# Performance work log

Measured on AMD Instinct MI355X. Metric: run time of the kernel, lower is better.

The kernel has to match this reference:

```python
import jax, jax.numpy as jnp
import numpy as np

D_MODEL = 1024
H = 16
T = 1024
B = 8

def setup_inputs() -> dict:
    key = jax.random.key(0)
    k0, k1, k2, k3, k4 = jax.random.split(key, 5)
    return {
        "x": jax.random.normal(k0, (B, T, D_MODEL), dtype=jnp.float32),
        "Wq": jax.random.normal(k1, (D_MODEL, D_MODEL), dtype=jnp.float32),
        "Wk": jax.random.normal(k2, (D_MODEL, D_MODEL), dtype=jnp.float32),
        "Wv": jax.random.normal(k3, (D_MODEL, D_MODEL), dtype=jnp.float32),
        "Wp": jax.random.normal(k4, (D_MODEL, D_MODEL), dtype=jnp.float32),
    }

def reference(x, Wq, Wk, Wv, Wp):
    b, t, d = x.shape
    dh = d // H
    # projections
    q = (x @ Wq).reshape(b, t, H, dh)
    k = (x @ Wk).reshape(b, t, H, dh)
    v = (x @ Wv).reshape(b, t, H, dh)
    # [b, h, t, t] attention scores, scaled by sqrt(d_head)
    scores = jnp.einsum("bqhd,bkhd->bhqk", q, k) / jnp.sqrt(jnp.float32(dh))
    attn = jax.nn.softmax(scores, axis=-1)
    # [b, h, t, dh] -> [b, t, d]
    out = jnp.einsum("bhqk,bkhd->bqhd", attn, v).reshape(b, t, d)
    return out @ Wp
```

## Files before the change

### kernel.cpp

```cpp
#include <hip/hip_runtime.h>
#include <math.h>


typedef unsigned short u16;
typedef unsigned int u32;
typedef __bf16  bf16x8 __attribute__((ext_vector_type(8)));
typedef unsigned short u16x8 __attribute__((ext_vector_type(8)));
typedef unsigned short u16x4 __attribute__((ext_vector_type(4)));
typedef short s16x4 __attribute__((ext_vector_type(4)));
typedef unsigned int u32x2 __attribute__((ext_vector_type(2)));
typedef float f32x4 __attribute__((ext_vector_type(4)));

#define MFMA16(a,b,c) __builtin_amdgcn_mfma_f32_16x16x32_bf16((a),(b),(c),0,0,0)
#define MFMA16K16(a,b,c) __builtin_amdgcn_mfma_f32_16x16x16bf16_1k((a),(b),(c),0,0,0)

static __device__ __forceinline__ u16 f2b(float f){
  unsigned u = __builtin_bit_cast(unsigned, f);
  u += 0x7fffu + ((u >> 16) & 1u);
  return (u16)(u >> 16);
}
static __device__ __forceinline__ float b2f(u16 h){
  unsigned u = ((unsigned)h) << 16;
  return __builtin_bit_cast(float, u);
}
static __device__ __forceinline__ bf16x8 ldsfrag(const u16* p){
  return __builtin_bit_cast(bf16x8, *(const u16x8*)p);
}
static __device__ __forceinline__ u32 packhi(float fa, float fb){
  return __builtin_amdgcn_perm(__builtin_bit_cast(u32, fa),
                               __builtin_bit_cast(u32, fb), 0x07060302u);
}
static __device__ __forceinline__ void gld16(const void* g, void* l){
  __builtin_amdgcn_global_load_lds(
      (const __attribute__((address_space(1))) void*)g,
      (__attribute__((address_space(3))) void*)l, 16, 0, 0);
}


__global__ __launch_bounds__(256) void split_x_kernel(
    const float* __restrict__ x, u16* __restrict__ xh, u16* __restrict__ xl, int n)
{
  int i = (blockIdx.x * 256 + threadIdx.x) * 8;
  if (i >= n) return;
  float4 v0 = *(const float4*)(x + i);
  float4 v1 = *(const float4*)(x + i + 4);
  float vv[8] = {v0.x, v0.y, v0.z, v0.w, v1.x, v1.y, v1.z, v1.w};
  u16x8 hv, lv;
#pragma unroll
  for (int j = 0; j < 8; j++){
    u16 hb = f2b(vv[j]);
    hv[j] = hb;
    lv[j] = f2b(vv[j] - b2f(hb));
  }
  *(u16x8*)(xh + i) = hv;
  *(u16x8*)(xl + i) = lv;
}

__global__ __launch_bounds__(256) void transpose4_kernel(
    const float* __restrict__ Wq, const float* __restrict__ Wk,
    const float* __restrict__ Wv, const float* __restrict__ Wp,
    u16* __restrict__ qh_, u16* __restrict__ ql_,
    u16* __restrict__ kh_, u16* __restrict__ kl_,
    u16* __restrict__ vt_, u16* __restrict__ pt_)
{
  __shared__ float t[32][33];
  const int z = blockIdx.z;
  const float* W = (z == 0) ? Wq : (z == 1) ? Wk : (z == 2) ? Wv : Wp;
  u16* Th = (z == 0) ? qh_ : (z == 1) ? kh_ : (z == 2) ? vt_ : pt_;
  u16* Tl = (z == 0) ? ql_ : (z == 1) ? kl_ : nullptr;
  int n0 = blockIdx.x * 32, k0 = blockIdx.y * 32;
  int tx = threadIdx.x, ty = threadIdx.y;
#pragma unroll
  for (int i = 0; i < 4; i++){
    int k = k0 + ty + i * 8;
    t[ty + i * 8][tx] = W[(size_t)k * 1024 + n0 + tx];
  }
  __syncthreads();
#pragma unroll
  for (int i = 0; i < 4; i++){
    int n = n0 + ty + i * 8;
    float v = t[tx][ty + i * 8];
    u16 h = f2b(v);
    Th[(size_t)n * 1024 + k0 + tx] = h;
    if (Tl) Tl[(size_t)n * 1024 + k0 + tx] = f2b(v - b2f(h));
  }
}

template<int OUTMODE>
__global__ __launch_bounds__(256) void gemm_bt_kernel(
    const u16* __restrict__ A, const u16* __restrict__ Bt, void* __restrict__ Cv,
    int M, int N, int K)
{
  __shared__ __attribute__((aligned(16))) u16 lA[4096], lB[4096];
  const int tid = threadIdx.x, lane = tid & 63, wave = tid >> 6;
  const int quad = lane >> 4, l15 = lane & 15;
  const int row0 = blockIdx.x * 128, col0 = blockIdx.y * 128;
  const int wm = wave >> 1, wn = wave & 1;
  const int sr = lane >> 2, sc = (lane & 3) * 8;
  f32x4 acc[4][4];
#pragma unroll
  for (int mt = 0; mt < 4; mt++)
#pragma unroll
    for (int nt = 0; nt < 4; nt++) acc[mt][nt] = (f32x4)0.0f;

  for (int k0 = 0; k0 < K; k0 += 32){
#pragma unroll
    for (int i = 0; i < 2; i++){
      int c = wave * 2 + i;
      gld16(A  + (size_t)(row0 + c * 16 + sr) * K + k0 + sc, &lA[c * 512]);
      gld16(Bt + (size_t)(col0 + c * 16 + sr) * K + k0 + sc, &lB[c * 512]);
    }
    __syncthreads();
    bf16x8 a[4], b[4];
#pragma unroll
    for (int t = 0; t < 4; t++){
      a[t] = ldsfrag(&lA[(wm * 64 + t * 16 + l15) * 32 + quad * 8]);
      b[t] = ldsfrag(&lB[(wn * 64 + t * 16 + l15) * 32 + quad * 8]);
    }
#pragma unroll
    for (int mt = 0; mt < 4; mt++)
#pragma unroll
      for (int nt = 0; nt < 4; nt++)
        acc[mt][nt] = MFMA16(a[mt], b[nt], acc[mt][nt]);
    __syncthreads();
  }
  if (OUTMODE == 2){
#pragma unroll
    for (int mt = 0; mt < 4; mt++)
#pragma unroll
      for (int nt = 0; nt < 4; nt++){
        int row = row0 + wm * 64 + mt * 16 + quad * 4;
        int col = col0 + wn * 64 + nt * 16 + l15;
        int bb = row >> 10, tt = row & 1023;
        int hh = (col >> 6) & 15, d = col & 63;
        int bhI = bb * 16 + hh;
        int ktile = tt >> 7, fkt = (tt >> 4) & 7, qF = (tt >> 2) & 3;
        int nd = d >> 4, l15F = d & 15;
        size_t idx = ((((size_t)(bhI * 8 + ktile) * 8 + fkt) * 4 + nd) * 64
                      + qF * 16 + l15F) * 4;
        u16x4 vals;
#pragma unroll
        for (int r = 0; r < 4; r++) vals[r] = f2b(acc[mt][nt][r]);
        *(u16x4*)(((u16*)Cv) + idx) = vals;
      }
  } else {
#pragma unroll
    for (int mt = 0; mt < 4; mt++)
#pragma unroll
      for (int nt = 0; nt < 4; nt++)
#pragma unroll
        for (int r = 0; r < 4; r++){
          int row = row0 + wm * 64 + mt * 16 + quad * 4 + r;
          int col = col0 + wn * 64 + nt * 16 + l15;
          ((float*)Cv)[(size_t)row * N + col] = acc[mt][nt][r];
        }
  }
}

__global__ __launch_bounds__(512, 2) void gemm_qk_kernel(
    const u16* __restrict__ Ah, const u16* __restrict__ Al,
    const u16* __restrict__ Bh, const u16* __restrict__ Bl,
    u16* __restrict__ Qhf, u16* __restrict__ Qlf,
    u16* __restrict__ Khf, u16* __restrict__ Klf, int M, int N, int K)
{
  __shared__ __attribute__((aligned(16))) u16 sA[2][2][8192], sB[2][2][8192];
  const int tid = threadIdx.x, lane = tid & 63, wave = tid >> 6;
  const int quad = lane >> 4, l15 = lane & 15;
  const int wm = wave >> 2, wn = wave & 3;
  const int row0 = blockIdx.x * 256, col0 = blockIdx.y * 256;
  const int f0a = (wave & 3) | ((wave & 4) << 1);
  const int f0b = (wave & 1) | ((wave >> 1) << 2);
  const size_t fstride = (size_t)16 * K;
  const size_t abase = (size_t)(row0 + l15) * K + quad * 8;
  const size_t bbase = (size_t)(col0 + l15) * K + quad * 8;
  (void)M; (void)N;

  f32x4 acc[8][4];
#pragma unroll
  for (int mt = 0; mt < 8; mt++)
#pragma unroll
    for (int nt = 0; nt < 4; nt++) acc[mt][nt] = (f32x4)0.0f;

#define STAGE_G0(KK, NB) do {                                              \
    gld16(Ah + abase + (size_t)f0a * fstride + (KK), &sA[NB][0][f0a * 512]); \
    gld16(Al + abase + (size_t)f0a * fstride + (KK), &sA[NB][1][f0a * 512]); \
    gld16(Bh + bbase + (size_t)f0b * fstride + (KK), &sB[NB][0][f0b * 512]); \
    gld16(Bl + bbase + (size_t)f0b * fstride + (KK), &sB[NB][1][f0b * 512]); \
  } while (0)
#define STAGE_G1(KK, NB) do {                                                        \
    gld16(Bh + bbase + (size_t)(f0b + 2) * fstride + (KK), &sB[NB][0][(f0b + 2) * 512]); \
    gld16(Bl + bbase + (size_t)(f0b + 2) * fstride + (KK), &sB[NB][1][(f0b + 2) * 512]); \
  } while (0)
#define STAGE_G2(KK, NB) do {                                                        \
    gld16(Ah + abase + (size_t)(f0a + 4) * fstride + (KK), &sA[NB][0][(f0a + 4) * 512]); \
    gld16(Al + abase + (size_t)(f0a + 4) * fstride + (KK), &sA[NB][1][(f0a + 4) * 512]); \
  } while (0)
#define RD_A(B4, BUF) do {                                        \
    _Pragma("unroll")                                             \
    for (int i = 0; i < 4; i++){                                  \
      int fa = wm * 8 + (B4) + i;                                 \
      ahf[i] = ldsfrag(&sA[BUF][0][fa * 512 + lane * 8]);         \
      alf[i] = ldsfrag(&sA[BUF][1][fa * 512 + lane * 8]);         \
    } } while (0)
#define RD_B(B2, BUF) do {                                        \
    _Pragma("unroll")                                             \
    for (int j = 0; j < 2; j++){                                  \
      int fb = wn * 4 + (B2) + j;                                 \
      bhf[j] = ldsfrag(&sB[BUF][0][fb * 512 + lane * 8]);         \
      blf[j] = ldsfrag(&sB[BUF][1][fb * 512 + lane * 8]);         \
    } } while (0)
#define MM(M0, N0) do {                                                      \
    __builtin_amdgcn_s_setprio(1);                                           \
    _Pragma("unroll")                                                        \
    for (int i = 0; i < 4; i++)                                              \
      _Pragma("unroll")                                                      \
      for (int j = 0; j < 2; j++){                                           \
        acc[(M0) + i][(N0) + j] = MFMA16(alf[i], bhf[j], acc[(M0) + i][(N0) + j]); \
        acc[(M0) + i][(N0) + j] = MFMA16(ahf[i], blf[j], acc[(M0) + i][(N0) + j]); \
        acc[(M0) + i][(N0) + j] = MFMA16(ahf[i], bhf[j], acc[(M0) + i][(N0) + j]); \
      }                                                                      \
    __builtin_amdgcn_s_setprio(0);                                           \
  } while (0)
#define VMCNT4() asm volatile("s_waitcnt vmcnt(4)" ::: "memory")
#define VMCNT6() asm volatile("s_waitcnt vmcnt(6)" ::: "memory")
#define BARRIER() asm volatile("s_barrier" ::: "memory")

  const int NT = K >> 5;
  STAGE_G0(0, 0);
  STAGE_G1(0, 0);
  STAGE_G2(0, 0);

  bf16x8 ahf[4], alf[4], bhf[2], blf[2];
#pragma unroll 2
  for (int t = 0; t < NT; t++){
    const int buf = t & 1, nb = buf ^ 1;
    const int kn = ((t + 1) & (NT - 1)) * 32;
    VMCNT4();
    BARRIER();
    RD_A(0, buf);
    RD_B(0, buf);
    STAGE_G0(kn, nb);
    MM(0, 0);
    VMCNT6();
    BARRIER();
    RD_B(2, buf);
    STAGE_G1(kn, nb);
    MM(0, 2);
    VMCNT6();
    BARRIER();
    RD_A(4, buf);
    STAGE_G2(kn, nb);
    MM(4, 2);
    RD_B(0, buf);
    MM(4, 0);
  }
  asm volatile("s_waitcnt vmcnt(0)" ::: "memory");

#undef STAGE_G0
#undef STAGE_G1
#undef STAGE_G2
#undef RD_A
#undef RD_B
#undef MM
#undef VMCNT4
#undef VMCNT6
#undef BARRIER

  const bool isQ = (col0 < 1024);
#pragma unroll
  for (int mt = 0; mt < 8; mt++)
#pragma unroll
    for (int nt = 0; nt < 4; nt++)
#pragma unroll
      for (int r = 0; r < 4; r++){
        int row = row0 + wm * 128 + mt * 16 + quad * 4 + r;
        int col = col0 + wn * 64 + nt * 16 + l15;
        int bb = row >> 10, tt = row & 1023;
        int hh = (col >> 6) & 15, d = col & 63;
        int bhI = bb * 16 + hh;
        int kc = d >> 5, qF = (d >> 3) & 3, j = d & 7;
        float v = acc[mt][nt][r];
        u16 hi = f2b(v);
        u16 lo = f2b(v - b2f(hi));
        if (isQ){
          int qtile = tt >> 7, rr = tt & 127;
          int wv = rr >> 5, mtF = (rr >> 4) & 1, l15F = tt & 15;
          size_t idx = ((((size_t)(bhI * 8 + qtile) * 4 + wv) * 2 + mtF) * 2 + kc) * 512
                       + (qF * 16 + l15F) * 8 + j;
          Qhf[idx] = hi; Qlf[idx] = lo;
        } else {
          int ktile = tt >> 7, fkt = (tt >> 4) & 7, l15F = tt & 15;
          size_t idx = (((size_t)(bhI * 8 + ktile) * 8 + fkt) * 2 + kc) * 512
                       + (qF * 16 + l15F) * 8 + j;
          Khf[idx] = hi; Klf[idx] = lo;
        }
      }
}

__global__ __launch_bounds__(256, 3) void attn_kernel(
    const u16* __restrict__ Qhf, const u16* __restrict__ Qlf,
    const u16* __restrict__ Khf, const u16* __restrict__ Klf,
    const u16* __restrict__ Vf, u16* __restrict__ O)
{
  __shared__ __attribute__((aligned(16))) u16 lKh[2][4096], lKl[2][4096], lV[2][4096];
  const int tid = threadIdx.x, lane = tid & 63, wave = tid >> 6;
  const int quad = lane >> 4, l15 = lane & 15;
  const int qt = blockIdx.x >> 7, bh = blockIdx.x & 127;
  const int b = bh >> 4, h = bh & 15;
  const int q0 = qt * 128;
  const float BETA = 0.18033688011112042f;

  bf16x8 qh[2][2], ql[2][2];
  {
    size_t qbase = (size_t)(bh * 8 + qt) * 8192 + wave * 2048 + lane * 8;
    u16* sh = &lKh[0][0];  u16* sl = &lKl[0][0];
#pragma unroll
    for (int i = 0; i < 4; i++){
      gld16(Qhf + qbase + i * 512, sh + wave * 2048 + i * 512);
      gld16(Qlf + qbase + i * 512, sl + wave * 2048 + i * 512);
    }
    __syncthreads();
#pragma unroll
    for (int mt = 0; mt < 2; mt++)
#pragma unroll
      for (int kc = 0; kc < 2; kc++){
        int off = wave * 2048 + (mt * 2 + kc) * 512 + lane * 8;
        qh[mt][kc] = ldsfrag(sh + off);
        ql[mt][kc] = ldsfrag(sl + off);
      }
    __syncthreads();
  }

  float m_i[2] = {-3.0e38f, -3.0e38f}, l_i[2] = {0.0f, 0.0f};
  f32x4 o_acc[2][4];
#pragma unroll
  for (int mt = 0; mt < 2; mt++)
#pragma unroll
    for (int nd = 0; nd < 4; nd++) o_acc[mt][nd] = (f32x4)0.0f;

  const size_t pan = (size_t)bh * 65536;
#pragma unroll
  for (int i = 0; i < 2; i++){
    int c = wave * 2 + i;
    gld16(Khf + pan + c * 512 + lane * 8, &lKh[0][c * 512]);
    gld16(Klf + pan + c * 512 + lane * 8, &lKl[0][c * 512]);
    gld16(Vf  + pan + c * 512 + lane * 8, &lV [0][c * 512]);
  }

#pragma unroll 1
  for (int j = 0; j < 16; j++){
    const int cur = j & 1;
    __syncthreads();
    if (j < 15){
      size_t nb = pan + (size_t)(j + 1) * 4096;
      const int nxt = cur ^ 1;
#pragma unroll
      for (int i = 0; i < 2; i++){
        int c = wave * 2 + i;
        gld16(Khf + nb + c * 512 + lane * 8, &lKh[nxt][c * 512]);
        gld16(Klf + nb + c * 512 + lane * 8, &lKl[nxt][c * 512]);
        gld16(Vf  + nb + c * 512 + lane * 8, &lV [nxt][c * 512]);
      }
    }

    f32x4 s[2][4];
#pragma unroll
    for (int qt2 = 0; qt2 < 2; qt2++)
#pragma unroll
      for (int f4 = 0; f4 < 4; f4++) s[qt2][f4] = (f32x4)0.0f;
#pragma unroll
    for (int f4 = 0; f4 < 4; f4++){
      int aoff = f4 * 1024 + lane * 8;
      bf16x8 kh0 = ldsfrag(&lKh[cur][aoff]);
      bf16x8 kh1 = ldsfrag(&lKh[cur][aoff + 512]);
      bf16x8 kl0 = ldsfrag(&lKl[cur][aoff]);
      bf16x8 kl1 = ldsfrag(&lKl[cur][aoff + 512]);
#pragma unroll
      for (int qt2 = 0; qt2 < 2; qt2++){
        s[qt2][f4] = MFMA16(kl0, qh[qt2][0], s[qt2][f4]);
        s[qt2][f4] = MFMA16(kl1, qh[qt2][1], s[qt2][f4]);
        s[qt2][f4] = MFMA16(kh0, ql[qt2][0], s[qt2][f4]);
        s[qt2][f4] = MFMA16(kh1, ql[qt2][1], s[qt2][f4]);
        s[qt2][f4] = MFMA16(kh0, qh[qt2][0], s[qt2][f4]);
        s[qt2][f4] = MFMA16(kh1, qh[qt2][1], s[qt2][f4]);
      }
    }

    float alpha[2];
#pragma unroll
    for (int qt2 = 0; qt2 < 2; qt2++){
      f32x4 mv = s[qt2][0];
#pragma unroll
      for (int f4 = 1; f4 < 4; f4++){
        mv[0] = fmaxf(mv[0], s[qt2][f4][0]); mv[1] = fmaxf(mv[1], s[qt2][f4][1]);
        mv[2] = fmaxf(mv[2], s[qt2][f4][2]); mv[3] = fmaxf(mv[3], s[qt2][f4][3]);
      }
      float mx = fmaxf(fmaxf(mv[0], mv[1]), fmaxf(mv[2], mv[3]));
      mx = fmaxf(mx, __shfl_xor(mx, 16));
      mx = fmaxf(mx, __shfl_xor(mx, 32));
      float mn = fmaxf(m_i[qt2], mx);
      alpha[qt2] = __builtin_amdgcn_exp2f((m_i[qt2] - mn) * BETA);
      m_i[qt2] = mn;
      float mb = mn * BETA;
      f32x4 ps = (f32x4)0.0f;
#pragma unroll
      for (int f4 = 0; f4 < 4; f4++)
#pragma unroll
        for (int r = 0; r < 4; r++){
          float p = __builtin_amdgcn_exp2f(s[qt2][f4][r] * BETA - mb);
          s[qt2][f4][r] = p;
          ps[r] += p;
        }
      float rs = (ps[0] + ps[1]) + (ps[2] + ps[3]);
      rs += __shfl_xor(rs, 16);
      rs += __shfl_xor(rs, 32);
      l_i[qt2] = l_i[qt2] * alpha[qt2] + rs;
    }

#pragma unroll
    for (int mt = 0; mt < 2; mt++)
#pragma unroll
      for (int r = 0; r < 4; r++){
        float ar = __shfl(alpha[mt], quad * 4 + r);
#pragma unroll
        for (int nd = 0; nd < 4; nd++) o_acc[mt][nd][r] *= ar;
      }

#pragma unroll
    for (int f4 = 0; f4 < 4; f4++){
      s16x4 vb[4];
#pragma unroll
      for (int nd = 0; nd < 4; nd++)
        vb[nd] = __builtin_bit_cast(s16x4,
                   *(const u16x4*)&lV[cur][(f4 * 4 + nd) * 256 + lane * 4]);
#pragma unroll
      for (int qt2 = 0; qt2 < 2; qt2++){
        u32x2 pd;
        pd[0] = packhi(s[qt2][f4][1], s[qt2][f4][0]);
        pd[1] = packhi(s[qt2][f4][3], s[qt2][f4][2]);
        s16x4 pa = __builtin_bit_cast(s16x4, pd);
#pragma unroll
        for (int nd = 0; nd < 4; nd++)
          o_acc[qt2][nd] = MFMA16K16(pa, vb[nd], o_acc[qt2][nd]);
      }
    }
  }

#pragma unroll
  for (int mt = 0; mt < 2; mt++)
#pragma unroll
    for (int r = 0; r < 4; r++){
      float lr = __shfl(l_i[mt], quad * 4 + r);
      float inv = 1.0f / lr;
      int t = q0 + wave * 32 + mt * 16 + quad * 4 + r;
      size_t rowoff = (size_t)(b * 1024 + t) * 1024 + h * 64;
#pragma unroll
      for (int nd = 0; nd < 4; nd++)
        O[rowoff + nd * 16 + l15] = f2b(o_acc[mt][nd][r] * inv);
    }
}

extern "C" void kernel_launch(void* const* d_in, const int* in_sizes, int n_in,
                              void* d_out, int out_size, void* d_ws, size_t ws_size,
                              hipStream_t stream)
{
  const float* x  = (const float*)d_in[0];
  const float* Wq = (const float*)d_in[1];
  const float* Wk = (const float*)d_in[2];
  const float* Wv = (const float*)d_in[3];
  const float* Wp = (const float*)d_in[4];
  float* out = (float*)d_out;
  char* ws = (char*)d_ws;
  const size_t MB = 1024 * 1024;
  u16* xh   = (u16*)(ws + 0);
  u16* xl   = (u16*)(ws + 16 * MB);
  u16* wqkh = (u16*)(ws + 32 * MB);
  u16* wqkl = (u16*)(ws + 36 * MB);
  u16* wvt  = (u16*)(ws + 40 * MB);
  u16* wpt  = (u16*)(ws + 42 * MB);
  u16* Qhf  = (u16*)(ws + 44 * MB);
  u16* Qlf  = (u16*)(ws + 60 * MB);
  u16* Khf  = (u16*)(ws + 76 * MB);
  u16* Klf  = (u16*)(ws + 92 * MB);
  u16* Vf   = (u16*)(ws + 108 * MB);
  u16* obuf = xh;
  (void)in_sizes; (void)n_in; (void)out_size; (void)ws_size;

  split_x_kernel<<<4096, 256, 0, stream>>>(x, xh, xl, 8 * 1024 * 1024);
  transpose4_kernel<<<dim3(32, 32, 4), dim3(32, 8), 0, stream>>>(
      Wq, Wk, Wv, Wp, wqkh, wqkl, wqkh + 1024 * 1024, wqkl + 1024 * 1024, wvt, wpt);
  gemm_qk_kernel<<<dim3(32, 8), 512, 0, stream>>>(xh, xl, wqkh, wqkl,
                                                  Qhf, Qlf, Khf, Klf, 8192, 2048, 1024);
  gemm_bt_kernel<2><<<dim3(64, 8), 256, 0, stream>>>(xh, wvt, (void*)Vf, 8192, 1024, 1024);
  attn_kernel<<<1024, 256, 0, stream>>>(Qhf, Qlf, Khf, Klf, Vf, obuf);
  gemm_bt_kernel<0><<<dim3(64, 8), 256, 0, stream>>>(obuf, wpt, (void*)out, 8192, 1024, 1024);
}
```

Measured before the change: 345.6 us.

## Restructure projection GEMM loop to one barrier and double-buffered register fragments

The three-phase staged K-loop, with partial vmcnt waits and three barriers per iteration, becomes a loop that waits for all global loads once, takes a single barrier, then issues every global-to-LDS copy for the next tile up front. A and B fragments now go into separate register sets, so LDS reads for the next sub-block can overlap the MFMAs of the current one. The aim is to cut barrier and wait overhead and improve MFMA/LDS overlap. The cost is higher VGPR pressure and coarser memory-latency hiding, since each iteration now waits for all outstanding loads.

```diff
diff --git a/kernel.cpp b/kernel.cpp
--- a/kernel.cpp
+++ b/kernel.cpp
@@ -181,90 +181,73 @@
 #pragma unroll
     for (int nt = 0; nt < 4; nt++) acc[mt][nt] = (f32x4)0.0f;
 
-#define STAGE_G0(KK, NB) do {                                              \
-    gld16(Ah + abase + (size_t)f0a * fstride + (KK), &sA[NB][0][f0a * 512]); \
-    gld16(Al + abase + (size_t)f0a * fstride + (KK), &sA[NB][1][f0a * 512]); \
-    gld16(Bh + bbase + (size_t)f0b * fstride + (KK), &sB[NB][0][f0b * 512]); \
-    gld16(Bl + bbase + (size_t)f0b * fstride + (KK), &sB[NB][1][f0b * 512]); \
-  } while (0)
-#define STAGE_G1(KK, NB) do {                                                        \
+#define STAGE_ALL(KK, NB) do {                                                           \
+    gld16(Ah + abase + (size_t)f0a * fstride + (KK), &sA[NB][0][f0a * 512]);             \
+    gld16(Al + abase + (size_t)f0a * fstride + (KK), &sA[NB][1][f0a * 512]);             \
+    gld16(Bh + bbase + (size_t)f0b * fstride + (KK), &sB[NB][0][f0b * 512]);             \
+    gld16(Bl + bbase + (size_t)f0b * fstride + (KK), &sB[NB][1][f0b * 512]);             \
     gld16(Bh + bbase + (size_t)(f0b + 2) * fstride + (KK), &sB[NB][0][(f0b + 2) * 512]); \
     gld16(Bl + bbase + (size_t)(f0b + 2) * fstride + (KK), &sB[NB][1][(f0b + 2) * 512]); \
-  } while (0)
-#define STAGE_G2(KK, NB) do {                                                        \
     gld16(Ah + abase + (size_t)(f0a + 4) * fstride + (KK), &sA[NB][0][(f0a + 4) * 512]); \
     gld16(Al + abase + (size_t)(f0a + 4) * fstride + (KK), &sA[NB][1][(f0a + 4) * 512]); \
   } while (0)
-#define RD_A(B4, BUF) do {                                        \
+#define RD_A2(DH, DL, B4, I0, BUF) do {                           \
     _Pragma("unroll")                                             \
-    for (int i = 0; i < 4; i++){                                  \
+    for (int i = (I0); i < (I0) + 2; i++){                        \
       int fa = wm * 8 + (B4) + i;                                 \
-      ahf[i] = ldsfrag(&sA[BUF][0][fa * 512 + lane * 8]);         \
-      alf[i] = ldsfrag(&sA[BUF][1][fa * 512 + lane * 8]);         \
+      DH[i] = ldsfrag(&sA[BUF][0][fa * 512 + lane * 8]);          \
+      DL[i] = ldsfrag(&sA[BUF][1][fa * 512 + lane * 8]);          \
     } } while (0)
-#define RD_B(B2, BUF) do {                                        \
+#define RD_B2(DH, DL, B2, BUF) do {                               \
     _Pragma("unroll")                                             \
     for (int j = 0; j < 2; j++){                                  \
       int fb = wn * 4 + (B2) + j;                                 \
-      bhf[j] = ldsfrag(&sB[BUF][0][fb * 512 + lane * 8]);         \
-      blf[j] = ldsfrag(&sB[BUF][1][fb * 512 + lane * 8]);         \
+      DH[j] = ldsfrag(&sB[BUF][0][fb * 512 + lane * 8]);          \
+      DL[j] = ldsfrag(&sB[BUF][1][fb * 512 + lane * 8]);          \
     } } while (0)
-#define MM(M0, N0) do {                                                      \
+#define MM(AH, AL, BH, BL, M0, N0) do {                                      \
     __builtin_amdgcn_s_setprio(1);                                           \
     _Pragma("unroll")                                                        \
     for (int i = 0; i < 4; i++)                                              \
       _Pragma("unroll")                                                      \
       for (int j = 0; j < 2; j++){                                           \
-        acc[(M0) + i][(N0) + j] = MFMA16(alf[i], bhf[j], acc[(M0) + i][(N0) + j]); \
-        acc[(M0) + i][(N0) + j] = MFMA16(ahf[i], blf[j], acc[(M0) + i][(N0) + j]); \
-        acc[(M0) + i][(N0) + j] = MFMA16(ahf[i], bhf[j], acc[(M0) + i][(N0) + j]); \
+        acc[(M0) + i][(N0) + j] = MFMA16(AL[i], BH[j], acc[(M0) + i][(N0) + j]); \
+        acc[(M0) + i][(N0) + j] = MFMA16(AH[i], BL[j], acc[(M0) + i][(N0) + j]); \
+        acc[(M0) + i][(N0) + j] = MFMA16(AH[i], BH[j], acc[(M0) + i][(N0) + j]); \
       }                                                                      \
     __builtin_amdgcn_s_setprio(0);                                           \
   } while (0)
-#define VMCNT4() asm volatile("s_waitcnt vmcnt(4)" ::: "memory")
-#define VMCNT6() asm volatile("s_waitcnt vmcnt(6)" ::: "memory")
-#define BARRIER() asm volatile("s_barrier" ::: "memory")
 
   const int NT = K >> 5;
-  STAGE_G0(0, 0);
-  STAGE_G1(0, 0);
-  STAGE_G2(0, 0);
-
-  bf16x8 ahf[4], alf[4], bhf[2], blf[2];
+  STAGE_ALL(0, 0);
+
+  bf16x8 a0h[4], a0l[4], a1h[4], a1l[4];
+  bf16x8 b0h[2], b0l[2], b1h[2], b1l[2];
 #pragma unroll 2
   for (int t = 0; t < NT; t++){
     const int buf = t & 1, nb = buf ^ 1;
     const int kn = ((t + 1) & (NT - 1)) * 32;
-    VMCNT4();
-    BARRIER();
-    RD_A(0, buf);
-    RD_B(0, buf);
-    STAGE_G0(kn, nb);
-    MM(0, 0);
-    VMCNT6();
-    BARRIER();
-    RD_B(2, buf);
-    STAGE_G1(kn, nb);
-    MM(0, 2);
-    VMCNT6();
-    BARRIER();
-    RD_A(4, buf);
-    STAGE_G2(kn, nb);
-    MM(4, 2);
-    RD_B(0, buf);
-    MM(4, 0);
+    asm volatile("s_waitcnt vmcnt(0)" ::: "memory");
+    asm volatile("s_barrier" ::: "memory");
+    STAGE_ALL(kn, nb);
+    RD_A2(a0h, a0l, 0, 0, buf);
+    RD_A2(a0h, a0l, 0, 2, buf);
+    RD_B2(b0h, b0l, 0, buf);
+    RD_B2(b1h, b1l, 2, buf);
+    MM(a0h, a0l, b0h, b0l, 0, 0);
+    RD_A2(a1h, a1l, 4, 0, buf);
+    MM(a0h, a0l, b1h, b1l, 0, 2);
+    RD_A2(a1h, a1l, 4, 2, buf);
+    RD_B2(b0h, b0l, 0, buf);
+    MM(a1h, a1l, b1h, b1l, 4, 2);
+    MM(a1h, a1l, b0h, b0l, 4, 0);
   }
   asm volatile("s_waitcnt vmcnt(0)" ::: "memory");
 
-#undef STAGE_G0
-#undef STAGE_G1
-#undef STAGE_G2
-#undef RD_A
-#undef RD_B
+#undef STAGE_ALL
+#undef RD_A2
+#undef RD_B2
 #undef MM
-#undef VMCNT4
-#undef VMCNT6
-#undef BARRIER
 
   const bool isQ = (col0 < 1024);
 #pragma unroll
```

New measurement: 350.7 us. About the same (+1.5%).
